# Performance work log

Measured on AMD Instinct MI355X. Metric: run time of the kernel, lower is better.

## Reference

```python
import jax, jax.numpy as jnp
import numpy as np

DIM, DIM_KQ, DIM_V, N = 1024, 64, 64, 8192

def setup_inputs() -> dict:
    key = jax.random.key(0)
    kx, kq, kk, kv = jax.random.split(key, 4)
    x = jax.random.normal(kx, (N, DIM), dtype=jnp.float32)
    # original uses torch.rand (uniform [0,1)) for parameter init
    w_q = jax.random.uniform(kq, (DIM, DIM_KQ), dtype=jnp.float32)
    w_k = jax.random.uniform(kk, (DIM, DIM_KQ), dtype=jnp.float32)
    w_v = jax.random.uniform(kv, (DIM, DIM_V), dtype=jnp.float32)
    return {"x": x, "w_q": w_q, "w_k": w_k, "w_v": w_v}

def reference(x, w_q, w_k, w_v):
    q = x @ w_q            # [N, dkq]
    k = x @ w_k            # [N, dkq]
    v = x @ w_v            # [N, dv]
    scale = 1.0 / jnp.sqrt(jnp.asarray(DIM_KQ, dtype=x.dtype))
    att_s = (q @ k.T) * scale           # [N, N]
    att_w = jax.nn.softmax(att_s, axis=-1)
    return att_w @ v                    # [N, dv]
```

## Files before the change

kernel.cpp:

```cpp
#include <hip/hip_runtime.h>
#include <hip/hip_bf16.h>
#include <math.h>

constexpr int N    = 8192;
constexpr int DIM  = 1024;

typedef __attribute__((ext_vector_type(8))) short bf16x8;
typedef __attribute__((ext_vector_type(4))) float f32x4;

__device__ inline unsigned short f2bf(float f) {
    unsigned u = __float_as_uint(f);
    u += 0x7fffu + ((u >> 16) & 1u);
    return (unsigned short)(u >> 16);
}
__device__ inline float bf2f(unsigned short h) {
    return __uint_as_float((unsigned)h << 16);
}
__device__ inline unsigned cvtpk(float a, float b) {
    unsigned r;
    asm("v_cvt_pk_bf16_f32 %0, %1, %2" : "=v"(r) : "v"(a), "v"(b));
    return r;
}
__device__ inline void gload16(const void* gsrc, void* ldst) {
    typedef __attribute__((address_space(1))) const unsigned int GU;
    typedef __attribute__((address_space(3))) unsigned int LU;
    __builtin_amdgcn_global_load_lds((GU*)gsrc, (LU*)ldst, 16, 0, 0);
}

__global__ __launch_bounds__(256) void prep_w_kernel(
    const float* __restrict__ wq, const float* __restrict__ wk,
    const float* __restrict__ wv,
    unsigned short* __restrict__ wthi, unsigned short* __restrict__ wtlo)
{
    int idx = blockIdx.x * 256 + threadIdx.x;
    int c   = idx >> 10;
    int k   = idx & 1023;
    const float* wsrc = (c < 64) ? wq : (c < 128) ? wk : wv;
    float f = wsrc[(size_t)k * 64 + (c & 63)];
    unsigned short h = f2bf(f);
    int pos = c * 1024 + (k & ~63) + ((((k >> 3) & 7) ^ (c & 7)) << 3) + (k & 7);
    wthi[pos] = h;
    wtlo[pos] = f2bf(f - bf2f(h));
}

__global__ __launch_bounds__(256) void proj_kernel(
    const float* __restrict__ x,
    const unsigned short* __restrict__ wthi,
    const unsigned short* __restrict__ wtlo,
    unsigned short* __restrict__ qhi, unsigned short* __restrict__ qlo,
    unsigned short* __restrict__ khi, unsigned short* __restrict__ klo,
    unsigned short* __restrict__ vthi)
{
    __shared__ unsigned short As[2][2][4096];
    __shared__ unsigned short Bs[2][2][3072];

    const int tid  = threadIdx.x;
    const int lane = tid & 63;
    const int w    = tid >> 6;
    const int g16  = lane >> 4;
    const int i16  = lane & 15;
    const int row0 = blockIdx.x * 64;
    const int col0 = blockIdx.y * 48;

    float4 xn[2][4];
    auto loadX = [&](int t, int s) {
#pragma unroll
        for (int i = 0; i < 4; ++i) {
            int f4 = i * 256 + tid;
            xn[s][i] = *reinterpret_cast<const float4*>(
                x + (size_t)(row0 + (f4 >> 4)) * DIM + t * 64 + (f4 & 15) * 4);
        }
    };
    auto stageB = [&](int t, int buf) {
#pragma unroll
        for (int i = 0; i < 3; ++i) {
            int idx = i * 256 + tid;
            int p   = (idx >= 384) ? 1 : 0;
            int li  = idx - p * 384;
            const unsigned short* base = p ? wtlo : wthi;
            const unsigned short* src  = base + (size_t)(col0 + (li >> 3)) * 1024
                                         + t * 64 + (li & 7) * 8;
            gload16(src, (char*)&Bs[buf][p][0] + (size_t)li * 16);
        }
    };
    auto writeA = [&](int buf, int s) {
#pragma unroll
        for (int i = 0; i < 4; ++i) {
            int f4 = i * 256 + tid;
            int r = f4 >> 4, c4 = f4 & 15;
            float4 v = xn[s][i];
            unsigned h01 = cvtpk(v.x, v.y);
            unsigned h23 = cvtpk(v.z, v.w);
            float hx = __uint_as_float(h01 << 16);
            float hy = __uint_as_float(h01 & 0xffff0000u);
            float hz = __uint_as_float(h23 << 16);
            float hw = __uint_as_float(h23 & 0xffff0000u);
            uint2 uh = { h01, h23 };
            uint2 ul = { cvtpk(v.x - hx, v.y - hy), cvtpk(v.z - hz, v.w - hw) };
            int byte = r * 128 + (((c4 >> 1) ^ (r & 7)) << 4) + ((c4 & 1) << 3);
            *reinterpret_cast<uint2*>((char*)&As[buf][0][0] + byte) = uh;
            *reinterpret_cast<uint2*>((char*)&As[buf][1][0] + byte) = ul;
        }
    };

    f32x4 acc[3];
    acc[0] = acc[1] = acc[2] = (f32x4){0.f, 0.f, 0.f, 0.f};

    loadX(0, 0);
    loadX(1, 1);
    stageB(0, 0);
    writeA(0, 0);

    const int arow = w * 16 + i16;
#pragma unroll
    for (int t = 0; t < 16; ++t) {
        const int b = t & 1;
        __syncthreads();
        if (t < 15) stageB(t + 1, b ^ 1);
        if (t < 14) loadX(t + 2, b);
        bf16x8 ah[2], al[2];
#pragma unroll
        for (int kc = 0; kc < 2; ++kc) {
            int off = arow * 128 + ((((kc << 2) | g16) ^ (arow & 7)) << 4);
            ah[kc] = *reinterpret_cast<const bf16x8*>((char*)&As[b][0][0] + off);
            al[kc] = *reinterpret_cast<const bf16x8*>((char*)&As[b][1][0] + off);
        }
#pragma unroll
        for (int ct = 0; ct < 3; ++ct) {
            const int colL = ct * 16 + i16;
#pragma unroll
            for (int kc = 0; kc < 2; ++kc) {
                int off = colL * 128 + ((((kc << 2) | g16) ^ (colL & 7)) << 4);
                bf16x8 bh = *reinterpret_cast<const bf16x8*>((char*)&Bs[b][0][0] + off);
                bf16x8 bl = *reinterpret_cast<const bf16x8*>((char*)&Bs[b][1][0] + off);
                acc[ct] = __builtin_amdgcn_mfma_f32_16x16x32_bf16(ah[kc], bh, acc[ct], 0, 0, 0);
                acc[ct] = __builtin_amdgcn_mfma_f32_16x16x32_bf16(ah[kc], bl, acc[ct], 0, 0, 0);
                acc[ct] = __builtin_amdgcn_mfma_f32_16x16x32_bf16(al[kc], bh, acc[ct], 0, 0, 0);
            }
        }
        if (t < 15) writeA(b ^ 1, b ^ 1);
    }

    const float QSCALE = 0.180336880f;
#pragma unroll
    for (int ct = 0; ct < 3; ++ct) {
        int cglob = col0 + ct * 16 + i16;
        int g = cglob >> 6, c64 = cglob & 63;
#pragma unroll
        for (int rr = 0; rr < 4; ++rr) {
            int row = row0 + w * 16 + 4 * g16 + rr;
            float f = acc[ct][rr];
            if (g == 0) {
                f *= QSCALE;
                unsigned short h = f2bf(f);
                qhi[(size_t)row * 64 + c64] = h;
                qlo[(size_t)row * 64 + c64] = f2bf(f - bf2f(h));
            } else if (g == 1) {
                int ci = c64 ^ ((row & 7) << 3);
                unsigned short h = f2bf(f);
                khi[(size_t)row * 64 + ci] = h;
                klo[(size_t)row * 64 + ci] = f2bf(f - bf2f(h));
            } else {
                int cg  = row >> 3;
                int cgs = (cg & ~7) | ((cg & 7) ^ (c64 & 7));
                vthi[(size_t)c64 * 8192 + cgs * 8 + (row & 7)] = f2bf(f);
            }
        }
    }
}

constexpr int BQ = 64;
constexpr int BK = 64;

__global__ __launch_bounds__(256) void attn_kernel(
    const unsigned short* __restrict__ qhi, const unsigned short* __restrict__ qlo,
    const unsigned short* __restrict__ khi, const unsigned short* __restrict__ klo,
    const unsigned short* __restrict__ vthi,
    float* __restrict__ po, float* __restrict__ pm, float* __restrict__ pl,
    int keys_per_split)
{
    __shared__ __align__(16) unsigned short stage[12288];
    __shared__ __align__(16) unsigned short plds[4][1024];

    const int tid  = threadIdx.x;
    const int lane = tid & 63;
    const int w    = tid >> 6;
    const int g16  = lane >> 4;
    const int i16  = lane & 15;
    const int qrow0 = blockIdx.x * BQ;
    const int split = blockIdx.y;
    const int key0  = split * keys_per_split;
    const int nt    = keys_per_split / BK;

    bf16x8 qh[2], ql[2];
    {
        const size_t qr = (size_t)(qrow0 + w * 16 + i16) * 64;
#pragma unroll
        for (int c = 0; c < 2; ++c) {
            qh[c] = *reinterpret_cast<const bf16x8*>(qhi + qr + c * 32 + g16 * 8);
            ql[c] = *reinterpret_cast<const bf16x8*>(qlo + qr + c * 32 + g16 * 8);
        }
    }

    float m = -INFINITY;
    float l = 0.f;
    f32x4 o_acc[4];
#pragma unroll
    for (int db = 0; db < 4; ++db) o_acc[db] = {0.f, 0.f, 0.f, 0.f};

    char* pb = (char*)&plds[w][0];
    const int wbase = i16 * 128;

    for (int t = 0; t < nt; ++t) {
        const int key0t = key0 + t * BK;
        __syncthreads();
#pragma unroll
        for (int u = 0; u < 6; ++u) {
            int row = ((u & 1) << 5) + (tid >> 3);
            int ch  = tid & 7;
            const unsigned short* src;
            if (u < 2)      src = khi  + (size_t)(key0t + row) * 64 + ch * 8;
            else if (u < 4) src = klo  + (size_t)(key0t + row) * 64 + ch * 8;
            else            src = vthi + (size_t)row * 8192 + key0t + ch * 8;
            gload16(src, (char*)stage + u * 4096 + tid * 16);
        }
        __syncthreads();
        const char* stg = (const char*)stage;

        f32x4 sacc[4];
#pragma unroll
        for (int j = 0; j < 4; ++j) {
            f32x4 a = {0.f, 0.f, 0.f, 0.f};
            const int kr = 16 * j + i16;
#pragma unroll
            for (int c = 0; c < 2; ++c) {
                const int byteO = kr * 128 + ((c * 64 + g16 * 16) ^ ((kr & 7) << 4));
                bf16x8 kh = *reinterpret_cast<const bf16x8*>(stg + byteO);
                bf16x8 kl = *reinterpret_cast<const bf16x8*>(stg + byteO + 8192);
                a = __builtin_amdgcn_mfma_f32_16x16x32_bf16(kh, qh[c], a, 0, 0, 0);
                a = __builtin_amdgcn_mfma_f32_16x16x32_bf16(kh, ql[c], a, 0, 0, 0);
                a = __builtin_amdgcn_mfma_f32_16x16x32_bf16(kl, qh[c], a, 0, 0, 0);
            }
            sacc[j] = a;
        }

        float a0 = fmaxf(fmaxf(sacc[0][0], sacc[0][1]), fmaxf(sacc[0][2], sacc[0][3]));
        float a1 = fmaxf(fmaxf(sacc[1][0], sacc[1][1]), fmaxf(sacc[1][2], sacc[1][3]));
        float a2 = fmaxf(fmaxf(sacc[2][0], sacc[2][1]), fmaxf(sacc[2][2], sacc[2][3]));
        float a3 = fmaxf(fmaxf(sacc[3][0], sacc[3][1]), fmaxf(sacc[3][2], sacc[3][3]));
        float aloc = fmaxf(fmaxf(a0, a1), fmaxf(a2, a3));
        if (__any(aloc > m + 8.f)) {
            float x2 = fmaxf(aloc, __shfl_xor(aloc, 16));
            x2 = fmaxf(x2, __shfl_xor(x2, 32));
            float mn   = fmaxf(m, x2);
            float corr = exp2f(m - mn);
            m = mn;
            l *= corr;
#pragma unroll
            for (int db = 0; db < 4; ++db) o_acc[db] *= corr;
        }

#pragma unroll
        for (int j = 0; j < 4; ++j) {
            float p0 = exp2f(sacc[j][0] - m);
            float p1 = exp2f(sacc[j][1] - m);
            float p2 = exp2f(sacc[j][2] - m);
            float p3 = exp2f(sacc[j][3] - m);
            l += (p0 + p1) + (p2 + p3);
            uint2 pdw = { cvtpk(p0, p1), cvtpk(p2, p3) };
            int off = wbase + ((32 * j + 8 * g16) ^ ((i16 & 7) << 4));
            *reinterpret_cast<uint2*>(pb + off) = pdw;
        }

        bf16x8 pfrag[2];
#pragma unroll
        for (int c = 0; c < 2; ++c) {
            int off = wbase + ((64 * c + 16 * g16) ^ ((i16 & 7) << 4));
            pfrag[c] = *reinterpret_cast<const bf16x8*>(pb + off);
        }
#pragma unroll
        for (int db = 0; db < 4; ++db) {
            f32x4 a = o_acc[db];
            const int vr = 16 * db + i16;
#pragma unroll
            for (int c = 0; c < 2; ++c) {
                const int byteO = 16384 + vr * 128 +
                                  ((c * 64 + g16 * 16) ^ ((vr & 7) << 4));
                bf16x8 vh = *reinterpret_cast<const bf16x8*>(stg + byteO);
                a = __builtin_amdgcn_mfma_f32_16x16x32_bf16(vh, pfrag[c], a, 0, 0, 0);
            }
            o_acc[db] = a;
        }
    }

    l += __shfl_xor(l, 16);
    l += __shfl_xor(l, 32);
    const size_t prow = (size_t)split * N + qrow0 + w * 16;
#pragma unroll
    for (int db = 0; db < 4; ++db) {
        float4 ov = {o_acc[db][0], o_acc[db][1], o_acc[db][2], o_acc[db][3]};
        *reinterpret_cast<float4*>(po + (prow + i16) * 64 + 16 * db + 4 * g16) = ov;
    }
    if (lane < 16) {
        pm[prow + i16] = m;
        pl[prow + i16] = l;
    }
}

__global__ __launch_bounds__(256) void combine_kernel(
    const float* __restrict__ po,
    const float* __restrict__ pm,
    const float* __restrict__ pl,
    float* __restrict__ out, int ns)
{
    const int tid = threadIdx.x;
    const int row = blockIdx.x * 16 + (tid >> 4);
    const int c4  = tid & 15;

    float M = -INFINITY;
    for (int s = 0; s < ns; ++s)
        M = fmaxf(M, pm[(size_t)s * N + row]);
    float L = 0.f;
    float4 acc = {0.f, 0.f, 0.f, 0.f};
    for (int s = 0; s < ns; ++s) {
        float ws = exp2f(pm[(size_t)s * N + row] - M);
        L += ws * pl[(size_t)s * N + row];
        float4 ov = *reinterpret_cast<const float4*>(
            po + ((size_t)s * N + row) * 64 + c4 * 4);
        acc.x += ws * ov.x; acc.y += ws * ov.y;
        acc.z += ws * ov.z; acc.w += ws * ov.w;
    }
    float inv = 1.f / L;
    float4 res = {acc.x * inv, acc.y * inv, acc.z * inv, acc.w * inv};
    *reinterpret_cast<float4*>(out + (size_t)row * 64 + c4 * 4) = res;
}

extern "C" void kernel_launch(void* const* d_in, const int* in_sizes, int n_in,
                              void* d_out, int out_size, void* d_ws, size_t ws_size,
                              hipStream_t stream)
{
    const float* x  = (const float*)d_in[0];
    const float* wq = (const float*)d_in[1];
    const float* wk = (const float*)d_in[2];
    const float* wv = (const float*)d_in[3];
    float* out = (float*)d_out;

    const size_t PLANE = (size_t)N * 64;
    unsigned short* qhi  = (unsigned short*)d_ws;
    unsigned short* qlo  = qhi + PLANE;
    unsigned short* khi  = qlo + PLANE;
    unsigned short* klo  = khi + PLANE;
    unsigned short* vthi = klo + PLANE;
    const size_t plane_bytes = 5 * PLANE * 2;
    const size_t wt_elems = (size_t)192 * 1024;
    const size_t wt_bytes = 2 * wt_elems * 2;

    int ns = 8;
    while (ns > 1 &&
           plane_bytes + wt_bytes +
           (size_t)ns * ((size_t)N * 64 * 4 + (size_t)N * 8) > ws_size)
        ns >>= 1;

    float* po = (float*)((char*)d_ws + plane_bytes);
    float* pm = po + (size_t)ns * N * 64;
    float* pl = pm + (size_t)ns * N;
    unsigned short* wthi = (unsigned short*)(pl + (size_t)ns * N);
    unsigned short* wtlo = wthi + wt_elems;

    prep_w_kernel<<<768, 256, 0, stream>>>(wq, wk, wv, wthi, wtlo);

    dim3 pgrid(N / 64, 4);
    proj_kernel<<<pgrid, 256, 0, stream>>>(x, wthi, wtlo,
                                           qhi, qlo, khi, klo, vthi);

    dim3 agrid(N / BQ, ns);
    attn_kernel<<<agrid, 256, 0, stream>>>(qhi, qlo, khi, klo, vthi,
                                           po, pm, pl, N / ns);

    combine_kernel<<<N / 16, 256, 0, stream>>>(po, pm, pl, out, ns);
}
```

Baseline: 85.39 us.

## Process two query sub-tiles per wave and compute row sums via MFMA

Doubles the query block to 128 rows so each wave handles two 16-row query slices. Each staged K/V tile in LDS is then reused across twice as many queries, which halves the global staging traffic per query and the number of blocks. The softmax denominator is now accumulated with an MFMA against a ones vector, computed from the same bf16-rounded probabilities, instead of scalar adds plus shuffles. In exchange the kernel uses more registers and LDS and launches fewer blocks, which may reduce occupancy and grid fill.

```diff
diff --git a/kernel.cpp b/kernel.cpp
--- a/kernel.cpp
+++ b/kernel.cpp
@@ -169,7 +169,7 @@
     }
 }
 
-constexpr int BQ = 64;
+constexpr int BQ = 128;
 constexpr int BK = 64;
 
 __global__ __launch_bounds__(256) void attn_kernel(
@@ -180,7 +180,7 @@
     int keys_per_split)
 {
     __shared__ __align__(16) unsigned short stage[12288];
-    __shared__ __align__(16) unsigned short plds[4][1024];
+    __shared__ __align__(16) unsigned short plds[4][2][1024];
 
     const int tid  = threadIdx.x;
     const int lane = tid & 63;
@@ -191,25 +191,31 @@
     const int split = blockIdx.y;
     const int key0  = split * keys_per_split;
     const int nt    = keys_per_split / BK;
-
-    bf16x8 qh[2], ql[2];
-    {
-        const size_t qr = (size_t)(qrow0 + w * 16 + i16) * 64;
+    const int xorm  = (i16 & 7) << 4;
+    const int wbase = i16 * 128;
+
+    bf16x8 qh[2][2], ql[2][2];
+#pragma unroll
+    for (int s = 0; s < 2; ++s) {
+        const size_t qr = (size_t)(qrow0 + w * 32 + s * 16 + i16) * 64;
 #pragma unroll
         for (int c = 0; c < 2; ++c) {
-            qh[c] = *reinterpret_cast<const bf16x8*>(qhi + qr + c * 32 + g16 * 8);
-            ql[c] = *reinterpret_cast<const bf16x8*>(qlo + qr + c * 32 + g16 * 8);
-        }
-    }
-
-    float m = -INFINITY;
-    float l = 0.f;
-    f32x4 o_acc[4];
-#pragma unroll
-    for (int db = 0; db < 4; ++db) o_acc[db] = {0.f, 0.f, 0.f, 0.f};
-
-    char* pb = (char*)&plds[w][0];
-    const int wbase = i16 * 128;
+            qh[s][c] = *reinterpret_cast<const bf16x8*>(qhi + qr + c * 32 + g16 * 8);
+            ql[s][c] = *reinterpret_cast<const bf16x8*>(qlo + qr + c * 32 + g16 * 8);
+        }
+    }
+    bf16x8 ones;
+#pragma unroll
+    for (int e = 0; e < 8; ++e) ones[e] = (short)0x3F80;
+
+    float m[2] = {-INFINITY, -INFINITY};
+    f32x4 o_acc[2][4], o5[2];
+#pragma unroll
+    for (int s = 0; s < 2; ++s) {
+        o5[s] = {0.f, 0.f, 0.f, 0.f};
+#pragma unroll
+        for (int db = 0; db < 4; ++db) o_acc[s][db] = {0.f, 0.f, 0.f, 0.f};
+    }
 
     for (int t = 0; t < nt; ++t) {
         const int key0t = key0 + t * BK;
@@ -227,83 +233,100 @@
         __syncthreads();
         const char* stg = (const char*)stage;
 
-        f32x4 sacc[4];
+        f32x4 sacc[2][4];
 #pragma unroll
         for (int j = 0; j < 4; ++j) {
-            f32x4 a = {0.f, 0.f, 0.f, 0.f};
+            sacc[0][j] = {0.f, 0.f, 0.f, 0.f};
+            sacc[1][j] = {0.f, 0.f, 0.f, 0.f};
             const int kr = 16 * j + i16;
 #pragma unroll
             for (int c = 0; c < 2; ++c) {
                 const int byteO = kr * 128 + ((c * 64 + g16 * 16) ^ ((kr & 7) << 4));
                 bf16x8 kh = *reinterpret_cast<const bf16x8*>(stg + byteO);
                 bf16x8 kl = *reinterpret_cast<const bf16x8*>(stg + byteO + 8192);
-                a = __builtin_amdgcn_mfma_f32_16x16x32_bf16(kh, qh[c], a, 0, 0, 0);
-                a = __builtin_amdgcn_mfma_f32_16x16x32_bf16(kh, ql[c], a, 0, 0, 0);
-                a = __builtin_amdgcn_mfma_f32_16x16x32_bf16(kl, qh[c], a, 0, 0, 0);
-            }
-            sacc[j] = a;
-        }
-
-        float a0 = fmaxf(fmaxf(sacc[0][0], sacc[0][1]), fmaxf(sacc[0][2], sacc[0][3]));
-        float a1 = fmaxf(fmaxf(sacc[1][0], sacc[1][1]), fmaxf(sacc[1][2], sacc[1][3]));
-        float a2 = fmaxf(fmaxf(sacc[2][0], sacc[2][1]), fmaxf(sacc[2][2], sacc[2][3]));
-        float a3 = fmaxf(fmaxf(sacc[3][0], sacc[3][1]), fmaxf(sacc[3][2], sacc[3][3]));
-        float aloc = fmaxf(fmaxf(a0, a1), fmaxf(a2, a3));
-        if (__any(aloc > m + 8.f)) {
-            float x2 = fmaxf(aloc, __shfl_xor(aloc, 16));
-            x2 = fmaxf(x2, __shfl_xor(x2, 32));
-            float mn   = fmaxf(m, x2);
-            float corr = exp2f(m - mn);
-            m = mn;
-            l *= corr;
-#pragma unroll
-            for (int db = 0; db < 4; ++db) o_acc[db] *= corr;
-        }
-
-#pragma unroll
-        for (int j = 0; j < 4; ++j) {
-            float p0 = exp2f(sacc[j][0] - m);
-            float p1 = exp2f(sacc[j][1] - m);
-            float p2 = exp2f(sacc[j][2] - m);
-            float p3 = exp2f(sacc[j][3] - m);
-            l += (p0 + p1) + (p2 + p3);
-            uint2 pdw = { cvtpk(p0, p1), cvtpk(p2, p3) };
-            int off = wbase + ((32 * j + 8 * g16) ^ ((i16 & 7) << 4));
-            *reinterpret_cast<uint2*>(pb + off) = pdw;
-        }
-
-        bf16x8 pfrag[2];
-#pragma unroll
-        for (int c = 0; c < 2; ++c) {
-            int off = wbase + ((64 * c + 16 * g16) ^ ((i16 & 7) << 4));
-            pfrag[c] = *reinterpret_cast<const bf16x8*>(pb + off);
-        }
+#pragma unroll
+                for (int s = 0; s < 2; ++s) {
+                    sacc[s][j] = __builtin_amdgcn_mfma_f32_16x16x32_bf16(kh, qh[s][c], sacc[s][j], 0, 0, 0);
+                    sacc[s][j] = __builtin_amdgcn_mfma_f32_16x16x32_bf16(kh, ql[s][c], sacc[s][j], 0, 0, 0);
+                    sacc[s][j] = __builtin_amdgcn_mfma_f32_16x16x32_bf16(kl, qh[s][c], sacc[s][j], 0, 0, 0);
+                }
+            }
+        }
+
+        float aloc[2];
+#pragma unroll
+        for (int s = 0; s < 2; ++s) {
+            float a0 = fmaxf(fmaxf(sacc[s][0][0], sacc[s][0][1]), fmaxf(sacc[s][0][2], sacc[s][0][3]));
+            float a1 = fmaxf(fmaxf(sacc[s][1][0], sacc[s][1][1]), fmaxf(sacc[s][1][2], sacc[s][1][3]));
+            float a2 = fmaxf(fmaxf(sacc[s][2][0], sacc[s][2][1]), fmaxf(sacc[s][2][2], sacc[s][2][3]));
+            float a3 = fmaxf(fmaxf(sacc[s][3][0], sacc[s][3][1]), fmaxf(sacc[s][3][2], sacc[s][3][3]));
+            aloc[s] = fmaxf(fmaxf(a0, a1), fmaxf(a2, a3));
+        }
+        int need = (aloc[0] > m[0] + 8.f) | (aloc[1] > m[1] + 8.f);
+        if (__any(need)) {
+#pragma unroll
+            for (int s = 0; s < 2; ++s) {
+                float x2 = fmaxf(aloc[s], __shfl_xor(aloc[s], 16));
+                x2 = fmaxf(x2, __shfl_xor(x2, 32));
+                float mn   = fmaxf(m[s], x2);
+                float corr = exp2f(m[s] - mn);
+                m[s] = mn;
+                o5[s] *= corr;
+#pragma unroll
+                for (int db = 0; db < 4; ++db) o_acc[s][db] *= corr;
+            }
+        }
+
+        bf16x8 pfrag[2][2];
+#pragma unroll
+        for (int s = 0; s < 2; ++s) {
+            char* pb = (char*)&plds[w][s][0];
+#pragma unroll
+            for (int j = 0; j < 4; ++j) {
+                float p0 = exp2f(sacc[s][j][0] - m[s]);
+                float p1 = exp2f(sacc[s][j][1] - m[s]);
+                float p2 = exp2f(sacc[s][j][2] - m[s]);
+                float p3 = exp2f(sacc[s][j][3] - m[s]);
+                uint2 pdw = { cvtpk(p0, p1), cvtpk(p2, p3) };
+                *reinterpret_cast<uint2*>(pb + wbase + ((32 * j + 8 * g16) ^ xorm)) = pdw;
+            }
+#pragma unroll
+            for (int c = 0; c < 2; ++c)
+                pfrag[s][c] = *reinterpret_cast<const bf16x8*>(
+                    pb + wbase + ((64 * c + 16 * g16) ^ xorm));
+            o5[s] = __builtin_amdgcn_mfma_f32_16x16x32_bf16(ones, pfrag[s][0], o5[s], 0, 0, 0);
+            o5[s] = __builtin_amdgcn_mfma_f32_16x16x32_bf16(ones, pfrag[s][1], o5[s], 0, 0, 0);
+        }
+
 #pragma unroll
         for (int db = 0; db < 4; ++db) {
-            f32x4 a = o_acc[db];
             const int vr = 16 * db + i16;
 #pragma unroll
             for (int c = 0; c < 2; ++c) {
                 const int byteO = 16384 + vr * 128 +
                                   ((c * 64 + g16 * 16) ^ ((vr & 7) << 4));
                 bf16x8 vh = *reinterpret_cast<const bf16x8*>(stg + byteO);
-                a = __builtin_amdgcn_mfma_f32_16x16x32_bf16(vh, pfrag[c], a, 0, 0, 0);
-            }
-            o_acc[db] = a;
-        }
-    }
-
-    l += __shfl_xor(l, 16);
-    l += __shfl_xor(l, 32);
-    const size_t prow = (size_t)split * N + qrow0 + w * 16;
-#pragma unroll
-    for (int db = 0; db < 4; ++db) {
-        float4 ov = {o_acc[db][0], o_acc[db][1], o_acc[db][2], o_acc[db][3]};
-        *reinterpret_cast<float4*>(po + (prow + i16) * 64 + 16 * db + 4 * g16) = ov;
-    }
-    if (lane < 16) {
-        pm[prow + i16] = m;
-        pl[prow + i16] = l;
+#pragma unroll
+                for (int s = 0; s < 2; ++s)
+                    o_acc[s][db] = __builtin_amdgcn_mfma_f32_16x16x32_bf16(
+                                       vh, pfrag[s][c], o_acc[s][db], 0, 0, 0);
+            }
+        }
+    }
+
+#pragma unroll
+    for (int s = 0; s < 2; ++s) {
+        const size_t prow = (size_t)split * N + qrow0 + w * 32 + s * 16;
+#pragma unroll
+        for (int db = 0; db < 4; ++db) {
+            float4 ov = {o_acc[s][db][0], o_acc[s][db][1],
+                         o_acc[s][db][2], o_acc[s][db][3]};
+            *reinterpret_cast<float4*>(po + (prow + i16) * 64 + 16 * db + 4 * g16) = ov;
+        }
+        if (lane < 16) {
+            pm[prow + i16] = m[s];
+            pl[prow + i16] = o5[s][0];
+        }
     }
 }
 
```

Result: no change. 84.80 us (-0.7%).
